# Kernel optimization log

Measured on AMD Instinct MI355X. Metric: run time of the kernel, lower is better.

The kernel has to match this reference:

```python
import jax, jax.numpy as jnp
import numpy as np

NUM_EXPERTS = 8
NUM_LANGS = 4
TOP_K = 2
D_MODEL = 1024
EXPERT_SIZE = 4096
B, S = 2, 2048


def setup_inputs() -> dict:
    key = jax.random.key(0)
    ks = jax.random.split(key, 6)
    def xavier(k, shape, fan_in, fan_out):
        a = float(np.sqrt(6.0 / (fan_in + fan_out)))
        return jax.random.uniform(k, shape, jnp.float32, -a, a)
    return {
        "x": jax.random.normal(ks[0], (B, S, D_MODEL), jnp.float32),
        "router_w": xavier(ks[1], (NUM_EXPERTS, D_MODEL), D_MODEL, NUM_EXPERTS),
        "router_b": jnp.zeros((NUM_EXPERTS,), jnp.float32),
        "lang_w": xavier(ks[2], (NUM_LANGS, D_MODEL), D_MODEL, NUM_LANGS),
        "lang_b": jnp.zeros((NUM_LANGS,), jnp.float32),
        "w1": xavier(ks[3], (NUM_EXPERTS, D_MODEL, EXPERT_SIZE), D_MODEL, EXPERT_SIZE),
        "b1": jnp.zeros((NUM_EXPERTS, EXPERT_SIZE), jnp.float32),
        "w2": xavier(ks[4], (NUM_EXPERTS, EXPERT_SIZE, D_MODEL), EXPERT_SIZE, D_MODEL),
        "b2": jnp.zeros((NUM_EXPERTS, D_MODEL), jnp.float32),
    }


def reference(x, router_w, router_b, lang_w, lang_b, w1, b1, w2, b2):
    # Language-aware routing bias
    lang_logits = x @ lang_w.T + lang_b                      # [B,S,L]
    lang_probs = jax.nn.softmax(lang_logits, axis=-1)
    # lang_probs[..., idx:idx+2].sum(-1): slice may be width 1 at the edge,
    # emulate with a zero pad column.
    lp_pad = jnp.pad(lang_probs, ((0, 0), (0, 0), (0, 1)))
    idx = jnp.arange(NUM_EXPERTS) % NUM_LANGS                # [E]
    expert_weights = lp_pad[..., idx] + lp_pad[..., idx + 1] # [B,S,E]

    router_logits = x @ router_w.T + router_b + 0.1 * expert_weights
    router_probs = jax.nn.softmax(router_logits, axis=-1)   # [B,S,E]
    top_p, top_i = jax.lax.top_k(router_probs, TOP_K)        # [B,S,K]
    top_p = top_p / top_p.sum(axis=-1, keepdims=True)

    # Dense per-expert MLP (dropout=0 / eval). torch GELU default = exact erf.
    h = jax.nn.gelu(jnp.einsum('bsd,edh->bseh', x, w1) + b1, approximate=False)
    expert_out = jnp.einsum('bseh,ehd->bsed', h, w2) + b2    # [B,S,E,D]

    sel = jnp.take_along_axis(expert_out, top_i[..., None], axis=2)  # [B,S,K,D]
    return (top_p[..., None] * sel).sum(axis=2)              # [B,S,D]
```

## Files before the change

kernel.cpp:

```cpp
#include <hip/hip_runtime.h>
#include <cstdint>
#include <cstddef>

#define T_TOK 4096
#define DM 1024
#define HS 4096
#define NE 8
#define MAXROWS 9216
#define MAXTILES 72

typedef __attribute__((ext_vector_type(8))) short short8;
typedef __attribute__((ext_vector_type(4))) float floatx4;

__device__ __forceinline__ unsigned short f2bf(float f) {
  union { float f; unsigned u; } v; v.f = f;
  unsigned r = (v.u + 0x7fffu + ((v.u >> 16) & 1u)) >> 16;
  return (unsigned short)r;
}

__device__ __forceinline__ void gload_lds16(const void* g, void* l) {
  __builtin_amdgcn_global_load_lds((const __attribute__((address_space(1))) void*)g,
                                   (__attribute__((address_space(3))) void*)l, 16, 0, 0);
}

__global__ void k_cvt_route(const float* __restrict__ x, unsigned short* __restrict__ xb,
                            const float* __restrict__ rw, const float* __restrict__ rb,
                            const float* __restrict__ lw, const float* __restrict__ lb,
                            int* __restrict__ top_i, float* __restrict__ top_p,
                            int* __restrict__ counts) {
#pragma unroll
  for (int j = 0; j < 4; j++) {
    int i = blockIdx.x * 1024 + j * 256 + threadIdx.x;
    float4 v = ((const float4*)x)[i];
    union { unsigned short us[4]; uint2 u2; } o;
    o.us[0] = f2bf(v.x); o.us[1] = f2bf(v.y); o.us[2] = f2bf(v.z); o.us[3] = f2bf(v.w);
    ((uint2*)xb)[i] = o.u2;
  }
  int t = blockIdx.x * 4 + (threadIdx.x >> 6);
  int lane = threadIdx.x & 63;
  const float4* xt = (const float4*)(x + (size_t)t * DM);
  float4 xv[4];
#pragma unroll
  for (int j = 0; j < 4; j++) xv[j] = xt[lane * 4 + j];
  float dots[12];
#pragma unroll
  for (int r = 0; r < 12; r++) {
    const float4* wr = (const float4*)(r < 4 ? lw + r * DM : rw + (r - 4) * DM);
    float s = 0.f;
#pragma unroll
    for (int j = 0; j < 4; j++) {
      float4 w = wr[lane * 4 + j];
      s += xv[j].x * w.x + xv[j].y * w.y + xv[j].z * w.z + xv[j].w * w.w;
    }
#pragma unroll
    for (int o = 32; o > 0; o >>= 1) s += __shfl_xor(s, o, 64);
    dots[r] = s;
  }
  if (lane == 0) {
    float lp[4]; float m = -1e30f;
#pragma unroll
    for (int i = 0; i < 4; i++) { lp[i] = dots[i] + lb[i]; m = fmaxf(m, lp[i]); }
    float sum = 0.f;
#pragma unroll
    for (int i = 0; i < 4; i++) { lp[i] = expf(lp[i] - m); sum += lp[i]; }
#pragma unroll
    for (int i = 0; i < 4; i++) lp[i] /= sum;
    float ew[4];
    ew[0] = lp[0] + lp[1]; ew[1] = lp[1] + lp[2]; ew[2] = lp[2] + lp[3]; ew[3] = lp[3];
    float r8[8];
#pragma unroll
    for (int e = 0; e < 8; e++) r8[e] = dots[4 + e] + rb[e] + 0.1f * ew[e & 3];
    int e0 = 0;
#pragma unroll
    for (int e = 1; e < 8; e++) if (r8[e] > r8[e0]) e0 = e;
    int e1 = (e0 == 0) ? 1 : 0;
#pragma unroll
    for (int e = 0; e < 8; e++) if (e != e0 && r8[e] > r8[e1]) e1 = e;
    float tt = expf(r8[e1] - r8[e0]);
    float w0 = 1.f / (1.f + tt);
    float w1 = tt / (1.f + tt);
    top_i[t * 2] = e0; top_i[t * 2 + 1] = e1;
    top_p[t * 2] = w0; top_p[t * 2 + 1] = w1;
    atomicAdd(&counts[e0], 1); atomicAdd(&counts[e1], 1);
  }
}

__global__ void k_offscatter(const int* __restrict__ counts, int* __restrict__ off,
                             const int* __restrict__ top_i, int* cursor,
                             unsigned* __restrict__ list) {
  if (threadIdx.x == 0) {
    int acc = 0;
    for (int e = 0; e < NE; e++) {
      off[e] = acc;
      acc += ((counts[e] + 127) >> 7) << 7;
    }
    off[NE] = acc;
  }
  __syncthreads();
  for (int t = threadIdx.x; t < T_TOK; t += 1024) {
#pragma unroll
    for (int k = 0; k < 2; k++) {
      int e = top_i[t * 2 + k];
      int pos = atomicAdd(&cursor[e], 1);
      list[off[e] + pos] = (unsigned)(t * 2 + k);
    }
  }
}

__global__ void k_transpose_bf16(const float* __restrict__ src, unsigned short* __restrict__ dst,
                                 int K, int N) {
  __shared__ float tile[64][65];
  const float* s = src + (size_t)blockIdx.z * K * N;
  unsigned short* d = dst + (size_t)blockIdx.z * K * N;
  int n0 = blockIdx.x * 64, k0 = blockIdx.y * 64;
  int tr = threadIdx.x >> 4;
  int tc = (threadIdx.x & 15) * 4;
#pragma unroll
  for (int j = 0; j < 4; j++) {
    int row = tr + j * 16;
    float4 v = *(const float4*)&s[(size_t)(k0 + row) * N + n0 + tc];
    tile[row][tc + 0] = v.x; tile[row][tc + 1] = v.y;
    tile[row][tc + 2] = v.z; tile[row][tc + 3] = v.w;
  }
  __syncthreads();
#pragma unroll
  for (int j = 0; j < 4; j++) {
    int n = tr + j * 16;
    union { unsigned short us[4]; uint2 u2; } o;
#pragma unroll
    for (int i = 0; i < 4; i++) o.us[i] = f2bf(tile[tc + i][n]);
    *(uint2*)&d[(size_t)(n0 + n) * K + k0 + tc] = o.u2;
  }
}

__global__ void k_init_out(const int* __restrict__ top_i, const float* __restrict__ top_p,
                           const float* __restrict__ b2, float* __restrict__ out) {
  int i = blockIdx.x * 256 + threadIdx.x;
  int t = i >> 10, d = i & 1023;
  int e0 = top_i[t * 2], e1 = top_i[t * 2 + 1];
  out[i] = top_p[t * 2] * b2[e0 * DM + d] + top_p[t * 2 + 1] * b2[e1 * DM + d];
}

__global__ __launch_bounds__(256, 4) void k_gemm1(
    const unsigned short* __restrict__ Abase,
    const unsigned short* __restrict__ Wt,
    const int* __restrict__ off, const unsigned* __restrict__ list,
    const float* __restrict__ bias, unsigned short* __restrict__ Hout) {
  const int K = DM, N = HS;
  int nx = gridDim.x;
  int flat = blockIdx.y * nx + blockIdx.x;
  int cpx = (nx * gridDim.y) >> 3;
  int swz = (flat & 7) * cpx + (flat >> 3);
  int n0 = (swz % nx) * 128;
  int r0 = (swz / nx) * 128;

  int total = off[NE];
  if (r0 >= total) return;
  int e = 0;
  while (r0 >= off[e + 1]) ++e;

  __shared__ __align__(16) unsigned short lB[2][128 * 32];

  int tid = threadIdx.x;
  int srow = tid >> 2;
  int key_s = (srow >> 1) & 3;
  int koff_src = ((tid & 3) ^ key_s) * 8;
  int kdst = (tid & 3) * 8;

  const unsigned short* srcB[2];
#pragma unroll
  for (int c = 0; c < 2; c++)
    srcB[c] = Wt + ((size_t)e * N + n0 + c * 64 + srow) * K + koff_src;

  int lane = tid & 63;
  int w = tid >> 6;
  int wm = w >> 1, wn = w & 1;
  int lr = lane & 15, kq = lane >> 4;
  int kx = kq ^ ((lr >> 1) & 3);

  unsigned aoff[4];
#pragma unroll
  for (int i = 0; i < 4; i++) {
    int row = r0 + wm * 64 + i * 16 + lr;
    unsigned pair = list[row];
    unsigned arow = (pair == 0xFFFFFFFFu) ? 0u : (pair >> 1);
    aoff[i] = arow * (unsigned)K + (unsigned)(kq * 8);
  }

  floatx4 acc[4][4] = {};

#define STAGEB(BUF, KK)                                                       \
  do {                                                                        \
    _Pragma("unroll")                                                         \
    for (int c = 0; c < 2; c++)                                               \
      gload_lds16(srcB[c] + (KK), &lB[BUF][(c * 64 + srow) * 32 + kdst]);     \
  } while (0)

  STAGEB(0, 0);
  __syncthreads();

  int cur = 0;
  for (int k0 = 0; k0 < K; k0 += 32) {
    if (k0 + 32 < K) STAGEB(cur ^ 1, k0 + 32);
    const short8* pB = (const short8*)lB[cur];
    short8 a[4], b[4];
#pragma unroll
    for (int i = 0; i < 4; i++)
      a[i] = *(const short8*)(Abase + aoff[i] + k0);
#pragma unroll
    for (int j = 0; j < 4; j++) b[j] = pB[(wn * 64 + j * 16 + lr) * 4 + kx];
#pragma unroll
    for (int i = 0; i < 4; i++)
#pragma unroll
      for (int j = 0; j < 4; j++)
        acc[i][j] = __builtin_amdgcn_mfma_f32_16x16x32_bf16(a[i], b[j], acc[i][j], 0, 0, 0);
    __syncthreads();
    cur ^= 1;
  }
#undef STAGEB

  int rbase = wm * 64 + kq * 4;
  int cbase = wn * 64 + lr;
#pragma unroll
  for (int i = 0; i < 4; i++)
#pragma unroll
    for (int j = 0; j < 4; j++)
#pragma unroll
      for (int g = 0; g < 4; g++) {
        int row = rbase + i * 16 + g;
        int col = cbase + j * 16;
        float v = acc[i][j][g] + bias[e * N + n0 + col];
        float u = v * (0.7978845608f + 0.0356774081f * v * v);
        float gl = v / (1.f + __expf(-2.f * u));
        Hout[(size_t)(r0 + row) * (size_t)N + n0 + col] = f2bf(gl);
      }
}

__global__ __launch_bounds__(256, 4) void k_gemm2(
    const unsigned short* __restrict__ Abase,
    const unsigned short* __restrict__ Wt,
    const int* __restrict__ off, const unsigned* __restrict__ list,
    const float* __restrict__ top_p, float* __restrict__ out) {
  const int K = HS, N = DM;
  int nx = gridDim.x;
  int flat = blockIdx.y * nx + blockIdx.x;
  int cpx = (nx * gridDim.y) >> 3;
  int swz = (flat & 7) * cpx + (flat >> 3);
  int n0 = (swz % nx) * 128;
  int r0 = (swz / nx) * 128;

  int total = off[NE];
  if (r0 >= total) return;
  int e = 0;
  while (r0 >= off[e + 1]) ++e;

  __shared__ __align__(16) unsigned short lA[2][128 * 32];
  __shared__ __align__(16) unsigned short lB[2][128 * 32];
  __shared__ float sP[128];
  __shared__ int sTok[128];

  int tid = threadIdx.x;
  int srow = tid >> 2;
  int key_s = (srow >> 1) & 3;
  int koff_src = ((tid & 3) ^ key_s) * 8;
  int kdst = (tid & 3) * 8;

  const unsigned short* srcA[2];
#pragma unroll
  for (int c = 0; c < 2; c++)
    srcA[c] = Abase + (size_t)(r0 + c * 64 + srow) * K + koff_src;
  const unsigned short* srcB[2];
#pragma unroll
  for (int c = 0; c < 2; c++)
    srcB[c] = Wt + ((size_t)e * N + n0 + c * 64 + srow) * K + koff_src;

  if (tid < 128) {
    unsigned pair = list[r0 + tid];
    if (pair == 0xFFFFFFFFu) { sTok[tid] = -1; sP[tid] = 0.f; }
    else { sTok[tid] = (int)(pair >> 1); sP[tid] = top_p[pair]; }
  }

  floatx4 acc[4][4] = {};
  int lane = tid & 63;
  int w = tid >> 6;
  int wm = w >> 1, wn = w & 1;
  int lr = lane & 15, kq = lane >> 4;
  int kx = kq ^ ((lr >> 1) & 3);

#define STAGE(BUF, KK)                                                        \
  do {                                                                        \
    _Pragma("unroll")                                                         \
    for (int c = 0; c < 2; c++) {                                             \
      gload_lds16(srcA[c] + (KK), &lA[BUF][(c * 64 + srow) * 32 + kdst]);     \
      gload_lds16(srcB[c] + (KK), &lB[BUF][(c * 64 + srow) * 32 + kdst]);     \
    }                                                                         \
  } while (0)

  STAGE(0, 0);
  __syncthreads();

  int cur = 0;
  for (int k0 = 0; k0 < K; k0 += 32) {
    if (k0 + 32 < K) STAGE(cur ^ 1, k0 + 32);
    const short8* pA = (const short8*)lA[cur];
    const short8* pB = (const short8*)lB[cur];
    short8 a[4], b[4];
#pragma unroll
    for (int i = 0; i < 4; i++) a[i] = pA[(wm * 64 + i * 16 + lr) * 4 + kx];
#pragma unroll
    for (int j = 0; j < 4; j++) b[j] = pB[(wn * 64 + j * 16 + lr) * 4 + kx];
#pragma unroll
    for (int i = 0; i < 4; i++)
#pragma unroll
      for (int j = 0; j < 4; j++)
        acc[i][j] = __builtin_amdgcn_mfma_f32_16x16x32_bf16(a[i], b[j], acc[i][j], 0, 0, 0);
    __syncthreads();
    cur ^= 1;
  }
#undef STAGE

  int rbase = wm * 64 + kq * 4;
  int cbase = wn * 64 + lr;
#pragma unroll
  for (int i = 0; i < 4; i++)
#pragma unroll
    for (int j = 0; j < 4; j++)
#pragma unroll
      for (int g = 0; g < 4; g++) {
        int row = rbase + i * 16 + g;
        int col = cbase + j * 16;
        int tok = sTok[row];
        if (tok >= 0)
          atomicAdd(&out[(size_t)tok * DM + n0 + col], sP[row] * acc[i][j][g]);
      }
}


extern "C" void kernel_launch(void* const* d_in, const int* in_sizes, int n_in,
                              void* d_out, int out_size, void* d_ws, size_t ws_size,
                              hipStream_t stream) {
  const float* x  = (const float*)d_in[0];
  const float* rw = (const float*)d_in[1];
  const float* rb = (const float*)d_in[2];
  const float* lw = (const float*)d_in[3];
  const float* lb = (const float*)d_in[4];
  const float* w1 = (const float*)d_in[5];
  const float* b1 = (const float*)d_in[6];
  const float* w2 = (const float*)d_in[7];
  const float* b2 = (const float*)d_in[8];
  float* out = (float*)d_out;
  char* ws = (char*)d_ws;

  int* counts = (int*)ws;
  int* cursor = (int*)(ws + 32);
  int* off    = (int*)(ws + 64);
  int* top_i  = (int*)(ws + 128);
  float* top_p = (float*)(ws + 128 + 32768);
  unsigned* list = (unsigned*)(ws + 65792);
  unsigned short* xb = (unsigned short*)(ws + 102912);
  unsigned short* wt = (unsigned short*)(ws + 102912 + 8388608);
  unsigned short* h  = (unsigned short*)(ws + 102912 + 8388608 + 67108864);

  hipMemsetAsync(ws, 0, 128, stream);
  hipMemsetAsync(list, 0xFF, MAXROWS * 4, stream);
  k_cvt_route<<<dim3(T_TOK / 4), dim3(256), 0, stream>>>(
      x, xb, rw, rb, lw, lb, top_i, top_p, counts);
  k_offscatter<<<dim3(1), dim3(1024), 0, stream>>>(counts, off, top_i, cursor, list);
  k_transpose_bf16<<<dim3(HS / 64, DM / 64, NE), dim3(256), 0, stream>>>(w1, wt, DM, HS);
  k_init_out<<<dim3(T_TOK * DM / 256), dim3(256), 0, stream>>>(top_i, top_p, b2, out);
  k_gemm1<<<dim3(HS / 128, MAXTILES), dim3(256), 0, stream>>>(
      xb, wt, off, list, b1, h);
  k_transpose_bf16<<<dim3(DM / 64, HS / 64, NE), dim3(256), 0, stream>>>(w2, wt, HS, DM);
  k_gemm2<<<dim3(DM / 128, MAXTILES), dim3(256), 0, stream>>>(
      h, wt, off, list, top_p, out);
}
```

Measured before the change: 583.9 us.

## Enlarge gemm1 to 256x256 tiles with LDS-staged gathered A and swizzle

Rewrites the first expert GEMM to use 256x256 output tiles with 512 threads and a K step of 64. The gathered token rows of A are now staged into LDS through direct global-to-LDS loads instead of being read straight from global memory into registers, and both operands use an XOR swizzle. MFMA issue is wrapped in setprio. Expert padding grows to 256 rows to match the new tile, which adds padded work and changes the tile counts of both GEMMs. The larger tile raises register and LDS use, leaving one block per CU.

After: 538.9 us. 1.08x faster.

```diff
diff --git a/kernel.cpp b/kernel.cpp
--- a/kernel.cpp
+++ b/kernel.cpp
@@ -6,8 +6,9 @@
 #define DM 1024
 #define HS 4096
 #define NE 8
-#define MAXROWS 9216
-#define MAXTILES 72
+#define MAXROWS 10240
+#define MT1 40
+#define MT2 80
 
 typedef __attribute__((ext_vector_type(8))) short short8;
 typedef __attribute__((ext_vector_type(4))) float floatx4;
@@ -92,7 +93,7 @@
     int acc = 0;
     for (int e = 0; e < NE; e++) {
       off[e] = acc;
-      acc += ((counts[e] + 127) >> 7) << 7;
+      acc += ((counts[e] + 255) >> 8) << 8;
     }
     off[NE] = acc;
   }
@@ -141,95 +142,101 @@
   out[i] = top_p[t * 2] * b2[e0 * DM + d] + top_p[t * 2 + 1] * b2[e1 * DM + d];
 }
 
-__global__ __launch_bounds__(256, 4) void k_gemm1(
+__global__ __launch_bounds__(512, 1) void k_gemm1(
     const unsigned short* __restrict__ Abase,
     const unsigned short* __restrict__ Wt,
     const int* __restrict__ off, const unsigned* __restrict__ list,
     const float* __restrict__ bias, unsigned short* __restrict__ Hout) {
-  const int K = DM, N = HS;
-  int nx = gridDim.x;
-  int flat = blockIdx.y * nx + blockIdx.x;
-  int cpx = (nx * gridDim.y) >> 3;
+  const int K = DM, N = HS, KT = DM / 64;
+  int gx = gridDim.x;
+  int flat = blockIdx.y * gx + blockIdx.x;
+  int cpx = (gx * gridDim.y) >> 3;
   int swz = (flat & 7) * cpx + (flat >> 3);
-  int n0 = (swz % nx) * 128;
-  int r0 = (swz / nx) * 128;
+  int n0 = (swz % gx) * 256;
+  int r0 = (swz / gx) * 256;
 
   int total = off[NE];
   if (r0 >= total) return;
   int e = 0;
   while (r0 >= off[e + 1]) ++e;
 
-  __shared__ __align__(16) unsigned short lB[2][128 * 32];
+  __shared__ __align__(16) unsigned short lA[2][256 * 64];
+  __shared__ __align__(16) unsigned short lB[2][256 * 64];
 
   int tid = threadIdx.x;
-  int srow = tid >> 2;
-  int key_s = (srow >> 1) & 3;
-  int koff_src = ((tid & 3) ^ key_s) * 8;
-  int kdst = (tid & 3) * 8;
-
-  const unsigned short* srcB[2];
-#pragma unroll
-  for (int c = 0; c < 2; c++)
-    srcB[c] = Wt + ((size_t)e * N + n0 + c * 64 + srow) * K + koff_src;
-
-  int lane = tid & 63;
-  int w = tid >> 6;
-  int wm = w >> 1, wn = w & 1;
+  int base = tid >> 3, c8 = tid & 7;
+  int koff = (c8 ^ (base & 7)) * 8;
+
+  unsigned aOff[4], bOff[4];
+#pragma unroll
+  for (int l = 0; l < 4; l++) {
+    int rowA = l * 64 + base;
+    unsigned pair = list[r0 + rowA];
+    unsigned arow = (pair == 0xFFFFFFFFu) ? 0u : (pair >> 1);
+    aOff[l] = arow * (unsigned)K + (unsigned)koff;
+    bOff[l] = (unsigned)(e * N + n0 + rowA) * (unsigned)K + (unsigned)koff;
+  }
+  int ldsb = base * 64 + c8 * 8;
+
+  int w = tid >> 6, lane = tid & 63;
+  int wm = w >> 2, wn = w & 3;
   int lr = lane & 15, kq = lane >> 4;
-  int kx = kq ^ ((lr >> 1) & 3);
-
-  unsigned aoff[4];
-#pragma unroll
-  for (int i = 0; i < 4; i++) {
-    int row = r0 + wm * 64 + i * 16 + lr;
-    unsigned pair = list[row];
-    unsigned arow = (pair == 0xFFFFFFFFu) ? 0u : (pair >> 1);
-    aoff[i] = arow * (unsigned)K + (unsigned)(kq * 8);
-  }
-
-  floatx4 acc[4][4] = {};
-
-#define STAGEB(BUF, KK)                                                       \
+  int rsel = lr & 7;
+
+  floatx4 acc[8][4] = {};
+
+#define STAGE1(BUF, TT)                                                       \
   do {                                                                        \
     _Pragma("unroll")                                                         \
-    for (int c = 0; c < 2; c++)                                               \
-      gload_lds16(srcB[c] + (KK), &lB[BUF][(c * 64 + srow) * 32 + kdst]);     \
+    for (int l = 0; l < 4; l++)                                               \
+      gload_lds16(Abase + aOff[l] + (TT) * 64, &lA[BUF][l * 4096 + ldsb]);    \
+    _Pragma("unroll")                                                         \
+    for (int l = 0; l < 4; l++)                                               \
+      gload_lds16(Wt + bOff[l] + (TT) * 64, &lB[BUF][l * 4096 + ldsb]);       \
   } while (0)
 
-  STAGEB(0, 0);
+  STAGE1(0, 0);
   __syncthreads();
 
   int cur = 0;
-  for (int k0 = 0; k0 < K; k0 += 32) {
-    if (k0 + 32 < K) STAGEB(cur ^ 1, k0 + 32);
-    const short8* pB = (const short8*)lB[cur];
-    short8 a[4], b[4];
-#pragma unroll
-    for (int i = 0; i < 4; i++)
-      a[i] = *(const short8*)(Abase + aoff[i] + k0);
-#pragma unroll
-    for (int j = 0; j < 4; j++) b[j] = pB[(wn * 64 + j * 16 + lr) * 4 + kx];
-#pragma unroll
-    for (int i = 0; i < 4; i++)
-#pragma unroll
-      for (int j = 0; j < 4; j++)
-        acc[i][j] = __builtin_amdgcn_mfma_f32_16x16x32_bf16(a[i], b[j], acc[i][j], 0, 0, 0);
+  for (int t = 0; t < KT; ++t) {
+    if (t + 1 < KT) STAGE1(cur ^ 1, t + 1);
+    const short8* qA = (const short8*)lA[cur];
+    const short8* qB = (const short8*)lB[cur];
+#pragma unroll
+    for (int kk = 0; kk < 2; kk++) {
+      short8 a[8], b[4];
+#pragma unroll
+      for (int m = 0; m < 8; m++)
+        a[m] = qA[(wm * 128 + m * 16 + lr) * 8 + ((kk * 4 + kq) ^ rsel)];
+#pragma unroll
+      for (int n = 0; n < 4; n++)
+        b[n] = qB[(wn * 64 + n * 16 + lr) * 8 + ((kk * 4 + kq) ^ rsel)];
+      __builtin_amdgcn_s_setprio(1);
+#pragma unroll
+      for (int m = 0; m < 8; m++)
+#pragma unroll
+        for (int n = 0; n < 4; n++)
+          acc[m][n] = __builtin_amdgcn_mfma_f32_16x16x32_bf16(a[m], b[n], acc[m][n], 0, 0, 0);
+      __builtin_amdgcn_s_setprio(0);
+    }
     __syncthreads();
     cur ^= 1;
   }
-#undef STAGEB
-
-  int rbase = wm * 64 + kq * 4;
-  int cbase = wn * 64 + lr;
-#pragma unroll
-  for (int i = 0; i < 4; i++)
-#pragma unroll
-    for (int j = 0; j < 4; j++)
+#undef STAGE1
+
+  float bcol[4];
+#pragma unroll
+  for (int n = 0; n < 4; n++) bcol[n] = bias[e * N + n0 + wn * 64 + n * 16 + lr];
+#pragma unroll
+  for (int m = 0; m < 8; m++)
+#pragma unroll
+    for (int n = 0; n < 4; n++)
 #pragma unroll
       for (int g = 0; g < 4; g++) {
-        int row = rbase + i * 16 + g;
-        int col = cbase + j * 16;
-        float v = acc[i][j][g] + bias[e * N + n0 + col];
+        int row = wm * 128 + m * 16 + kq * 4 + g;
+        int col = wn * 64 + n * 16 + lr;
+        float v = acc[m][n][g] + bcol[n];
         float u = v * (0.7978845608f + 0.0356774081f * v * v);
         float gl = v / (1.f + __expf(-2.f * u));
         Hout[(size_t)(r0 + row) * (size_t)N + n0 + col] = f2bf(gl);
@@ -287,7 +294,7 @@
   int lr = lane & 15, kq = lane >> 4;
   int kx = kq ^ ((lr >> 1) & 3);
 
-#define STAGE(BUF, KK)                                                        \
+#define STAGE2(BUF, KK)                                                       \
   do {                                                                        \
     _Pragma("unroll")                                                         \
     for (int c = 0; c < 2; c++) {                                             \
@@ -296,12 +303,12 @@
     }                                                                         \
   } while (0)
 
-  STAGE(0, 0);
+  STAGE2(0, 0);
   __syncthreads();
 
   int cur = 0;
   for (int k0 = 0; k0 < K; k0 += 32) {
-    if (k0 + 32 < K) STAGE(cur ^ 1, k0 + 32);
+    if (k0 + 32 < K) STAGE2(cur ^ 1, k0 + 32);
     const short8* pA = (const short8*)lA[cur];
     const short8* pB = (const short8*)lB[cur];
     short8 a[4], b[4];
@@ -317,7 +324,7 @@
     __syncthreads();
     cur ^= 1;
   }
-#undef STAGE
+#undef STAGE2
 
   int rbase = wm * 64 + kq * 4;
   int cbase = wn * 64 + lr;
@@ -356,10 +363,10 @@
   int* off    = (int*)(ws + 64);
   int* top_i  = (int*)(ws + 128);
   float* top_p = (float*)(ws + 128 + 32768);
-  unsigned* list = (unsigned*)(ws + 65792);
-  unsigned short* xb = (unsigned short*)(ws + 102912);
-  unsigned short* wt = (unsigned short*)(ws + 102912 + 8388608);
-  unsigned short* h  = (unsigned short*)(ws + 102912 + 8388608 + 67108864);
+  unsigned* list = (unsigned*)(ws + 128 + 65536);
+  unsigned short* xb = (unsigned short*)(ws + 131072);
+  unsigned short* wt = (unsigned short*)(ws + 131072 + 8388608);
+  unsigned short* h  = (unsigned short*)(ws + 131072 + 8388608 + 67108864);
 
   hipMemsetAsync(ws, 0, 128, stream);
   hipMemsetAsync(list, 0xFF, MAXROWS * 4, stream);
@@ -368,9 +375,9 @@
   k_offscatter<<<dim3(1), dim3(1024), 0, stream>>>(counts, off, top_i, cursor, list);
   k_transpose_bf16<<<dim3(HS / 64, DM / 64, NE), dim3(256), 0, stream>>>(w1, wt, DM, HS);
   k_init_out<<<dim3(T_TOK * DM / 256), dim3(256), 0, stream>>>(top_i, top_p, b2, out);
-  k_gemm1<<<dim3(HS / 128, MAXTILES), dim3(256), 0, stream>>>(
+  k_gemm1<<<dim3(HS / 256, MT1), dim3(512), 0, stream>>>(
       xb, wt, off, list, b1, h);
   k_transpose_bf16<<<dim3(DM / 64, HS / 64, NE), dim3(256), 0, stream>>>(w2, wt, HS, DM);
-  k_gemm2<<<dim3(DM / 128, MAXTILES), dim3(256), 0, stream>>>(
+  k_gemm2<<<dim3(DM / 128, MT2), dim3(256), 0, stream>>>(
       h, wt, off, list, top_p, out);
 }
```
